# Kernel tuning notes

Measured on AMD Instinct MI355X. Metric: run time of the kernel, lower is better.

The kernel has to match this reference:

```python
import jax, jax.numpy as jnp
import numpy as np

D_MODEL = 2048
N_HEADS = 16
HEAD_DIM = D_MODEL // N_HEADS  # 128
HIDDEN = int(8 * D_MODEL / 3)  # 5461
EPS = 1e-6


def setup_inputs() -> dict:
    key = jax.random.key(0)
    ks = jax.random.split(key, 12)
    B, S = 2, 2048
    std = D_MODEL ** -0.5
    return {
        "x": jax.random.normal(ks[0], (B, S, D_MODEL), jnp.float32),
        "freq_cis": jax.random.normal(ks[1], (S, HEAD_DIM // 2, 2, 2), jnp.float32),
        "wq": jax.random.normal(ks[2], (D_MODEL, D_MODEL), jnp.float32) * std,
        "wk": jax.random.normal(ks[3], (D_MODEL, D_MODEL), jnp.float32) * std,
        "wv": jax.random.normal(ks[4], (D_MODEL, D_MODEL), jnp.float32) * std,
        "wo": jax.random.normal(ks[5], (D_MODEL, D_MODEL), jnp.float32) * std,
        "bo": jnp.zeros((D_MODEL,), jnp.float32),
        "w1": jax.random.normal(ks[6], (HIDDEN, D_MODEL), jnp.float32) * std,
        "w3": jax.random.normal(ks[7], (HIDDEN, D_MODEL), jnp.float32) * std,
        "w2": jax.random.normal(ks[8], (D_MODEL, HIDDEN), jnp.float32) * (HIDDEN ** -0.5),
        "g_attn": jnp.ones((D_MODEL,), jnp.float32),
        "g_ffn": jnp.ones((D_MODEL,), jnp.float32),
    }


def rmsnorm(x, g):
    xf = x.astype(jnp.float32)
    return xf * jax.lax.rsqrt(jnp.mean(xf * xf, axis=-1, keepdims=True) + EPS) * g


def rope(xq, xk, f):
    # xq/xk: [b, s, h, hd]; f: [s, hd/2, 2, 2]
    b, s, h, hd = xq.shape
    xq_ = xq.reshape(b, s, h, hd // 2, 2)
    xk_ = xk.reshape(b, s, h, hd // 2, 2)
    # out[b,s,h,i,j] = sum_k x[b,s,h,i,k] * f[s,i,j,k]
    q = jnp.einsum("bshik,sijk->bshij", xq_, f).reshape(b, s, h, hd)
    k = jnp.einsum("bshik,sijk->bshij", xk_, f).reshape(b, s, h, hd)
    return q, k


def reference(x, freq_cis, wq, wk, wv, wo, bo, w1, w3, w2, g_attn, g_ffn):
    b, s, d = x.shape
    h, hd = N_HEADS, HEAD_DIM
    scale = hd ** -0.5

    # --- attention sublayer ---
    xn = rmsnorm(x, g_attn)
    q = jnp.einsum("bsd,ed->bse", xn, wq).reshape(b, s, h, hd)
    k = jnp.einsum("bsd,ed->bse", xn, wk).reshape(b, s, h, hd)
    v = jnp.einsum("bsd,ed->bse", xn, wv).reshape(b, s, h, hd)
    q, k = rope(q, k, freq_cis[:s])
    attn = jnp.einsum("bqhd,bkhd->bhqk", q, k) * scale
    attn = jax.nn.softmax(attn, axis=-1)
    o = jnp.einsum("bhqk,bkhd->bqhd", attn, v).reshape(b, s, d)
    o = jnp.einsum("bsd,ed->bse", o, wo) + bo
    hres = x + o

    # --- SwiGLU FFN sublayer ---
    hn = rmsnorm(hres, g_ffn)
    x1 = jnp.einsum("bsd,hd->bsh", hn, w1)
    x3 = jnp.einsum("bsd,hd->bsh", hn, w3)
    ffn = jnp.einsum("bsh,dh->bsd", jax.nn.silu(x1) * x3, w2)
    return hres + ffn
```

## Files before the change

kernel.cpp:

```cpp
#include <hip/hip_runtime.h>

#define D_MODEL 2048
#define NHEADS 16
#define HDIM 128
#define HIDDEN_ 5461
#define HP2 5632
#define BATCH 2
#define SEQ 2048
#define MTOK 4096

typedef unsigned short u16;
typedef __attribute__((ext_vector_type(8))) short bf16x8;
typedef __attribute__((ext_vector_type(4))) float f32x4;
typedef __attribute__((ext_vector_type(4))) short s16x4;

__device__ __forceinline__ u16 f2b(float f) {
  union { float f; unsigned u; } v; v.f = f;
  return (u16)((v.u + 0x7FFFu + ((v.u >> 16) & 1u)) >> 16);
}
__device__ __forceinline__ float b2f(u16 u) {
  union { unsigned u; float f; } v; v.u = ((unsigned)u) << 16;
  return v.f;
}
__device__ __forceinline__ void gload16(const void* g, void* l) {
  __builtin_amdgcn_global_load_lds(
      (const __attribute__((address_space(1))) unsigned int*)g,
      (__attribute__((address_space(3))) unsigned int*)l, 16, 0, 0);
}

#define SB0() __builtin_amdgcn_sched_barrier(0)
#define BARRIER() do { SB0(); __builtin_amdgcn_s_barrier(); SB0(); } while (0)
#define LGKM0() do { asm volatile("s_waitcnt lgkmcnt(0)" ::: "memory"); SB0(); } while (0)

__global__ __launch_bounds__(256) void k_conv8(const float* __restrict__ src,
                                               u16* __restrict__ dst, int n8) {
  int stride = gridDim.x * 256;
  for (int i = blockIdx.x * 256 + threadIdx.x; i < n8; i += stride) {
    const float4* s = (const float4*)src + (size_t)i * 2;
    float4 a = s[0], b = s[1];
    bf16x8 o;
    o[0] = f2b(a.x); o[1] = f2b(a.y); o[2] = f2b(a.z); o[3] = f2b(a.w);
    o[4] = f2b(b.x); o[5] = f2b(b.y); o[6] = f2b(b.z); o[7] = f2b(b.w);
    ((bf16x8*)dst)[i] = o;
  }
}

__global__ __launch_bounds__(256) void k_conv3(const float* __restrict__ s0,
                                               const float* __restrict__ s1,
                                               const float* __restrict__ s2,
                                               u16* __restrict__ dst) {
  const int n8 = D_MODEL * D_MODEL / 8;
  int total = 3 * n8;
  int stride = gridDim.x * 256;
  for (int i = blockIdx.x * 256 + threadIdx.x; i < total; i += stride) {
    int seg = i >> 19, j = i & (n8 - 1);
    const float* s = (seg == 0) ? s0 : (seg == 1 ? s1 : s2);
    const float4* sp = (const float4*)s + (size_t)j * 2;
    float4 a = sp[0], b = sp[1];
    bf16x8 o;
    o[0] = f2b(a.x); o[1] = f2b(a.y); o[2] = f2b(a.z); o[3] = f2b(a.w);
    o[4] = f2b(b.x); o[5] = f2b(b.y); o[6] = f2b(b.z); o[7] = f2b(b.w);
    ((bf16x8*)dst)[i] = o;
  }
}

__global__ __launch_bounds__(256) void k_convw13(const float* __restrict__ w1,
                                                 const float* __restrict__ w3,
                                                 u16* __restrict__ dst) {
  const int n8 = (11264 * D_MODEL) / 8;
  int stride = gridDim.x * 256;
  for (int i = blockIdx.x * 256 + threadIdx.x; i < n8; i += stride) {
    int r = i >> 8, c8 = i & 255;
    int t = r & 255;
    int srow = ((r >> 8) << 7) + (t & 127);
    bf16x8 o;
    if (srow < HIDDEN_) {
      const float* s = (t < 128) ? w1 : w3;
      const float4* sp = (const float4*)(s + (size_t)srow * D_MODEL + c8 * 8);
      float4 a = sp[0], b = sp[1];
      o[0] = f2b(a.x); o[1] = f2b(a.y); o[2] = f2b(a.z); o[3] = f2b(a.w);
      o[4] = f2b(b.x); o[5] = f2b(b.y); o[6] = f2b(b.z); o[7] = f2b(b.w);
    } else {
      o = (bf16x8){0, 0, 0, 0, 0, 0, 0, 0};
    }
    ((bf16x8*)dst)[i] = o;
  }
}

__global__ __launch_bounds__(256) void k_convpad(const float* __restrict__ src,
                                                 u16* __restrict__ dst,
                                                 int srows, int scols, int drows, int dcols) {
  size_t n = (size_t)drows * dcols;
  size_t stride = (size_t)gridDim.x * 256;
  for (size_t i = blockIdx.x * 256 + threadIdx.x; i < n; i += stride) {
    int r = (int)(i / dcols), c = (int)(i % dcols);
    float v = (r < srows && c < scols) ? src[(size_t)r * scols + c] : 0.f;
    dst[i] = f2b(v);
  }
}

__global__ __launch_bounds__(256) void k_rmsnorm(const float* __restrict__ X,
                                                 const float* __restrict__ G,
                                                 u16* __restrict__ Out) {
  int row = blockIdx.x;
  int tid = threadIdx.x;
  const float4* x4 = (const float4*)(X + (size_t)row * D_MODEL);
  float4 a = x4[tid * 2], b = x4[tid * 2 + 1];
  float ss = a.x * a.x + a.y * a.y + a.z * a.z + a.w * a.w +
             b.x * b.x + b.y * b.y + b.z * b.z + b.w * b.w;
#pragma unroll
  for (int off = 1; off < 64; off <<= 1) ss += __shfl_xor(ss, off);
  __shared__ float part[4];
  if ((tid & 63) == 0) part[tid >> 6] = ss;
  __syncthreads();
  float rstd = rsqrtf((part[0] + part[1] + part[2] + part[3]) * (1.0f / D_MODEL) + 1e-6f);
  const float4* g4 = (const float4*)G;
  float4 ga = g4[tid * 2], gb = g4[tid * 2 + 1];
  bf16x8 o;
  o[0] = f2b(a.x * rstd * ga.x); o[1] = f2b(a.y * rstd * ga.y);
  o[2] = f2b(a.z * rstd * ga.z); o[3] = f2b(a.w * rstd * ga.w);
  o[4] = f2b(b.x * rstd * gb.x); o[5] = f2b(b.y * rstd * gb.y);
  o[6] = f2b(b.z * rstd * gb.z); o[7] = f2b(b.w * rstd * gb.w);
  *((bf16x8*)(Out + (size_t)row * D_MODEL) + tid) = o;
}

template <int WN, int EPI>
__global__ __launch_bounds__(512, 2) void k_gemm2(const u16* __restrict__ A,
                                                  const u16* __restrict__ Bw,
                                                  const u16* __restrict__ Bw2,
                                                  void* __restrict__ O0,
                                                  void* __restrict__ O1,
                                                  void* __restrict__ O2,
                                                  const float* __restrict__ bias,
                                                  const float* __restrict__ res,
                                                  const u16* __restrict__ aux,
                                                  int M, int N, int K) {
  constexpr int BN = WN * 64;
  constexpr int PB = BN * 64;
  __shared__ __align__(128) char lds[65536 + 4 * PB];
  const int tid = threadIdx.x;
  const int w = tid >> 6, lane = tid & 63;
  const int lo = lane & 15, hi = lane >> 4;
  const int wr = w >> 2, wc = w & 3;

  const int ntN = N / BN;
  const int nwg = gridDim.x * gridDim.y;
  const int flat = blockIdx.y * gridDim.x + blockIdx.x;
  const int swz = (flat & 7) * (nwg >> 3) + (flat >> 3);
  const int tm = swz / ntN, tn = swz % ntN;
  const int m0 = tm * 256, n0 = tn * BN;

  const u16* bbase;
  if (EPI == 5)
    bbase = (n0 < 5632) ? Bw + (size_t)n0 * K : Bw2 + (size_t)(n0 - 5632) * K;
  else
    bbase = Bw + (size_t)n0 * K;

  auto stA = [&](int nb, int kk, int k0) {
#pragma unroll
    for (int j = 0; j < 2; ++j) {
      int row = j * 128 + (tid >> 2);
      const u16* g = A + (size_t)(m0 + row) * K + k0 + kk * 32 + (tid & 3) * 8;
      gload16(g, lds + nb * 32768 + kk * 16384 + j * 8192 + tid * 16);
    }
  };
  auto stB = [&](int nb, int kk, int k0) {
#pragma unroll
    for (int j = 0; j < WN / 2; ++j) {
      int row = j * 128 + (tid >> 2);
      const u16* g = bbase + (size_t)row * K + k0 + kk * 32 + (tid & 3) * 8;
      gload16(g, lds + 65536 + nb * 2 * PB + kk * PB + j * 8192 + tid * 16);
    }
  };
  auto ldA = [&](int buf, int kk, int mf) {
    return *(const bf16x8*)(lds + buf * 32768 + kk * 16384 +
                            (wr * 128 + mf * 16 + lo) * 64 + hi * 16);
  };
  auto ldB = [&](int buf, int kk, int nf) {
    return *(const bf16x8*)(lds + 65536 + buf * 2 * PB + kk * PB +
                            (wc * (WN * 16) + nf * 16 + lo) * 64 + hi * 16);
  };
#define VMCNT_CONFIRM()                                             \
  do {                                                              \
    if constexpr (WN == 4)                                          \
      asm volatile("s_waitcnt vmcnt(4)" ::: "memory");              \
    else                                                            \
      asm volatile("s_waitcnt vmcnt(3)" ::: "memory");              \
    SB0();                                                          \
  } while (0)

  f32x4 acc[8][WN];
#pragma unroll
  for (int i = 0; i < 8; i++)
#pragma unroll
    for (int j = 0; j < WN; j++) acc[i][j] = (f32x4){0.f, 0.f, 0.f, 0.f};

  stA(0, 0, 0);
  stB(0, 0, 0);
  stA(0, 1, 0);
  stB(0, 1, 0);
  VMCNT_CONFIRM();
  BARRIER();

  const int KT = K / 64;
  for (int kt = 0; kt < KT; ++kt) {
    const int buf = kt & 1, nb = buf ^ 1;
    int kn = (kt + 1) * 64;
    if (kn >= K) kn = 0;
    bf16x8 aF[4], bF[WN];

#pragma unroll
    for (int i = 0; i < 4; i++) aF[i] = ldA(buf, 0, i);
#pragma unroll
    for (int j = 0; j < WN; j++) bF[j] = ldB(buf, 0, j);
    stA(nb, 0, kn);
    BARRIER();
    LGKM0();
    __builtin_amdgcn_s_setprio(1);
#pragma unroll
    for (int i = 0; i < 4; i++)
#pragma unroll
      for (int j = 0; j < WN; j++)
        acc[i][j] = __builtin_amdgcn_mfma_f32_16x16x32_bf16(aF[i], bF[j], acc[i][j], 0, 0, 0);
    __builtin_amdgcn_s_setprio(0);
    BARRIER();

#pragma unroll
    for (int i = 0; i < 4; i++) aF[i] = ldA(buf, 0, 4 + i);
    stB(nb, 0, kn);
    VMCNT_CONFIRM();
    BARRIER();
    LGKM0();
    __builtin_amdgcn_s_setprio(1);
#pragma unroll
    for (int i = 0; i < 4; i++)
#pragma unroll
      for (int j = 0; j < WN; j++)
        acc[4 + i][j] = __builtin_amdgcn_mfma_f32_16x16x32_bf16(aF[i], bF[j], acc[4 + i][j], 0, 0, 0);
    __builtin_amdgcn_s_setprio(0);
    BARRIER();

#pragma unroll
    for (int i = 0; i < 4; i++) aF[i] = ldA(buf, 1, i);
#pragma unroll
    for (int j = 0; j < WN; j++) bF[j] = ldB(buf, 1, j);
    stA(nb, 1, kn);
    BARRIER();
    LGKM0();
    __builtin_amdgcn_s_setprio(1);
#pragma unroll
    for (int i = 0; i < 4; i++)
#pragma unroll
      for (int j = 0; j < WN; j++)
        acc[i][j] = __builtin_amdgcn_mfma_f32_16x16x32_bf16(aF[i], bF[j], acc[i][j], 0, 0, 0);
    __builtin_amdgcn_s_setprio(0);
    BARRIER();

#pragma unroll
    for (int i = 0; i < 4; i++) aF[i] = ldA(buf, 1, 4 + i);
    stB(nb, 1, kn);
    VMCNT_CONFIRM();
    BARRIER();
    LGKM0();
    __builtin_amdgcn_s_setprio(1);
#pragma unroll
    for (int i = 0; i < 4; i++)
#pragma unroll
      for (int j = 0; j < WN; j++)
        acc[4 + i][j] = __builtin_amdgcn_mfma_f32_16x16x32_bf16(aF[i], bF[j], acc[4 + i][j], 0, 0, 0);
    __builtin_amdgcn_s_setprio(0);
    BARRIER();
  }

  if (EPI == 6) {
    u16* xls = (u16*)lds;
    if (wc >= 2) {
#pragma unroll
      for (int i = 0; i < 8; i++)
#pragma unroll
        for (int j = 0; j < WN; j++) {
          int col = (wc - 2) * 64 + j * 16 + lo;
#pragma unroll
          for (int r = 0; r < 4; r++) {
            int row = wr * 128 + i * 16 + hi * 4 + r;
            xls[row * 132 + col] = f2b(acc[i][j][r]);
          }
        }
    }
    BARRIER();
    if (wc < 2) {
      int c0 = n0 >> 1;
#pragma unroll
      for (int i = 0; i < 8; i++)
#pragma unroll
        for (int j = 0; j < WN; j++) {
          int colL = wc * 64 + j * 16 + lo;
#pragma unroll
          for (int r = 0; r < 4; r++) {
            int rowL = wr * 128 + i * 16 + hi * 4 + r;
            float v1 = acc[i][j][r];
            float v3 = b2f(xls[rowL * 132 + colL]);
            float sig = 1.f / (1.f + __expf(-v1));
            ((u16*)O0)[(size_t)(m0 + rowL) * 5632 + c0 + colL] = f2b(v1 * sig * v3);
          }
        }
    }
    return;
  }
  u16* qkvout = nullptr;
  int c0 = 0;
  if (EPI == 1) {
    int seg = n0 >> 11;
    qkvout = (u16*)(seg == 0 ? O0 : (seg == 1 ? O1 : O2));
    c0 = n0 & 2047;
  }
  u16* w13out = nullptr;
  int w13c0 = 0;
  if (EPI == 5) {
    w13out = (u16*)(n0 < 5632 ? O0 : O1);
    w13c0 = (n0 < 5632) ? n0 : n0 - 5632;
  }
#pragma unroll
  for (int i = 0; i < 8; i++) {
#pragma unroll
    for (int j = 0; j < WN; j++) {
      int colL = wc * (WN * 16) + j * 16 + lo;
#pragma unroll
      for (int r = 0; r < 4; r++) {
        int row = m0 + wr * 128 + i * 16 + hi * 4 + r;
        float v = acc[i][j][r];
        if (EPI == 0) {
          ((u16*)O0)[(size_t)row * N + n0 + colL] = f2b(v);
        } else if (EPI == 1) {
          qkvout[(size_t)row * 2048 + c0 + colL] = f2b(v);
        } else if (EPI == 2) {
          size_t idx = (size_t)row * N + n0 + colL;
          ((float*)O0)[idx] = v + bias[n0 + colL] + res[idx];
        } else if (EPI == 3) {
          size_t idx = (size_t)row * N + n0 + colL;
          ((float*)O0)[idx] = v + res[idx];
        } else if (EPI == 5) {
          w13out[(size_t)row * 5632 + w13c0 + colL] = f2b(v);
        }
      }
    }
  }
#undef VMCNT_CONFIRM
}

__global__ __launch_bounds__(256) void k_rope(u16* __restrict__ Qb, u16* __restrict__ Kb,
                                              const float* __restrict__ F) {
  int n = MTOK * (D_MODEL / 2);
  int stride = gridDim.x * 256;
  for (int t = blockIdx.x * 256 + threadIdx.x; t < n; t += stride) {
    int i = t & 63;
    int rest = t >> 6;
    int hh = rest & 15;
    int tok = rest >> 4;
    int s = tok & (SEQ - 1);
    float4 f = ((const float4*)F)[s * 64 + i];
    size_t off = (size_t)tok * D_MODEL + hh * HDIM + i * 2;
    float x0 = b2f(Qb[off]), x1 = b2f(Qb[off + 1]);
    Qb[off] = f2b(x0 * f.x + x1 * f.y);
    Qb[off + 1] = f2b(x0 * f.z + x1 * f.w);
    x0 = b2f(Kb[off]); x1 = b2f(Kb[off + 1]);
    Kb[off] = f2b(x0 * f.x + x1 * f.y);
    Kb[off + 1] = f2b(x0 * f.z + x1 * f.w);
  }
}

__global__ __launch_bounds__(256) void k_vt(const u16* __restrict__ V, u16* __restrict__ VT) {
  __shared__ u16 t[64][72];
  const int stile = blockIdx.x;
  const int bh = blockIdx.y;
  const int dz = blockIdx.z;
  const int b = bh >> 4, h = bh & 15;
  const int tok0 = b * SEQ + stile * 64;
  const int d0 = dz * 64;
  const int tid = threadIdx.x;
#pragma unroll
  for (int p = 0; p < 2; p++) {
    int idx = p * 256 + tid;
    int row = idx >> 3, seg = idx & 7;
    bf16x8 v = *(const bf16x8*)(V + (size_t)(tok0 + row) * D_MODEL + h * HDIM + d0 + seg * 8);
    *(bf16x8*)(&t[row][seg * 8]) = v;
  }
  __syncthreads();
#pragma unroll
  for (int p = 0; p < 2; p++) {
    int idx = p * 256 + tid;
    int dr = idx >> 3, seg = idx & 7;
    bf16x8 o;
#pragma unroll
    for (int e = 0; e < 8; e++) o[e] = t[seg * 8 + e][dr];
    *(bf16x8*)(VT + ((size_t)bh * HDIM + d0 + dr) * SEQ + stile * 64 + seg * 8) = o;
  }
}

__global__ __launch_bounds__(256) void k_flash4(const u16* __restrict__ Q,
                                                const u16* __restrict__ Kb,
                                                const u16* __restrict__ VT,
                                                u16* __restrict__ O) {
  __shared__ u16 Kt[64 * 128];
  __shared__ u16 Vt[128 * 64];
  __shared__ u16 Pl[4][2][16 * 72];
  const int tid = threadIdx.x;
  const int w = tid >> 6, lane = tid & 63;
  const int lo = lane & 15, hi = lane >> 4;
  const int qt = blockIdx.x, bh = blockIdx.y;
  const int b = bh >> 4, h = bh & 15;
  const size_t qrow0 = (size_t)b * SEQ + qt * 128 + w * 32;
  const float SC = 0.08838834764831845f * 1.4426950408889634f;

  bf16x8 aQ[2][4];
#pragma unroll
  for (int qg = 0; qg < 2; qg++)
#pragma unroll
    for (int kb = 0; kb < 4; kb++)
      aQ[qg][kb] = *(const bf16x8*)(Q + (qrow0 + qg * 16 + lo) * D_MODEL + h * HDIM + kb * 32 + hi * 8);

  float m_s[2] = {-3.0e38f, -3.0e38f}, l_s[2] = {0.f, 0.f};
  f32x4 oacc[2][8];
#pragma unroll
  for (int qg = 0; qg < 2; qg++)
#pragma unroll
    for (int d = 0; d < 8; d++) oacc[qg][d] = (f32x4){0.f, 0.f, 0.f, 0.f};

  const int krowL = tid >> 4;
  const int kslot = (tid & 15) ^ (krowL & 7);
  const int vrowL = tid >> 3;
  const int vslot = (tid & 7) ^ (vrowL & 7);
  const u16* Kbase = Kb + (size_t)b * SEQ * D_MODEL + h * HDIM;
  const u16* Vbase = VT + (size_t)bh * HDIM * SEQ;
  unsigned* Plw = (unsigned*)&Pl[w][0][0];

  bf16x8 kreg[4], vreg[4];
  auto issue = [&](int kt) {
#pragma unroll
    for (int t = 0; t < 4; t++) {
      int row = t * 16 + krowL;
      kreg[t] = *(const bf16x8*)(Kbase + (size_t)(kt * 64 + row) * D_MODEL + kslot * 8);
    }
#pragma unroll
    for (int t = 0; t < 4; t++) {
      int row = t * 32 + vrowL;
      vreg[t] = *(const bf16x8*)(Vbase + (size_t)row * SEQ + kt * 64 + vslot * 8);
    }
  };
  auto commit = [&]() {
#pragma unroll
    for (int t = 0; t < 4; t++)
      *(bf16x8*)((char*)Kt + t * 4096 + tid * 16) = kreg[t];
#pragma unroll
    for (int t = 0; t < 4; t++)
      *(bf16x8*)((char*)Vt + t * 4096 + tid * 16) = vreg[t];
  };

  issue(0);
  commit();
  BARRIER();

  const int NT = SEQ / 64;
  for (int kt = 0; kt < NT; kt++) {
    if (kt + 1 < NT) {
      issue(kt + 1);
      SB0();
    }

    f32x4 sf[2][4];
#pragma unroll
    for (int cb = 0; cb < 4; cb++) {
      bf16x8 kA[4];
#pragma unroll
      for (int kb = 0; kb < 4; kb++) {
        int ps = (kb * 4 + hi) ^ (lo & 7);
        kA[kb] = *(const bf16x8*)(Kt + (cb * 16 + lo) * 128 + ps * 8);
      }
#pragma unroll
      for (int qg = 0; qg < 2; qg++) {
        f32x4 s = (f32x4){0.f, 0.f, 0.f, 0.f};
#pragma unroll
        for (int kb = 0; kb < 4; kb++)
          s = __builtin_amdgcn_mfma_f32_16x16x32_bf16(kA[kb], aQ[qg][kb], s, 0, 0, 0);
        sf[qg][cb] = s;
      }
    }

    float tsc[2];
    bool ok = true;
#pragma unroll
    for (int qg = 0; qg < 2; qg++) {
      float t0 = fmaxf(fmaxf(sf[qg][0][0], sf[qg][0][1]), fmaxf(sf[qg][0][2], sf[qg][0][3]));
      float t1 = fmaxf(fmaxf(sf[qg][1][0], sf[qg][1][1]), fmaxf(sf[qg][1][2], sf[qg][1][3]));
      float t2 = fmaxf(fmaxf(sf[qg][2][0], sf[qg][2][1]), fmaxf(sf[qg][2][2], sf[qg][2][3]));
      float t3 = fmaxf(fmaxf(sf[qg][3][0], sf[qg][3][1]), fmaxf(sf[qg][3][2], sf[qg][3][3]));
      float t = fmaxf(fmaxf(t0, t1), fmaxf(t2, t3));
      t = fmaxf(t, __shfl_xor(t, 16));
      t = fmaxf(t, __shfl_xor(t, 32));
      tsc[qg] = t * SC;
      ok = ok && (tsc[qg] - m_s[qg] <= 11.5f);
    }
    bool skip = __all(ok);
#pragma unroll
    for (int qg = 0; qg < 2; qg++) {
      float mm = m_s[qg];
      if (!skip) {
        mm = fmaxf(m_s[qg], tsc[qg]);
        float alpha = exp2f(m_s[qg] - mm);
        l_s[qg] *= alpha;
#pragma unroll
        for (int d = 0; d < 8; d++) oacc[qg][d] *= alpha;
        m_s[qg] = mm;
      }
      float rs = 0.f;
#pragma unroll
      for (int cb = 0; cb < 4; cb++) {
        float p0 = exp2f(sf[qg][cb][0] * SC - mm);
        float p1 = exp2f(sf[qg][cb][1] * SC - mm);
        float p2 = exp2f(sf[qg][cb][2] * SC - mm);
        float p3 = exp2f(sf[qg][cb][3] * SC - mm);
        rs += (p0 + p1) + (p2 + p3);
        unsigned pk0, pk1;
        asm("v_cvt_pk_bf16_f32 %0, %1, %2" : "=v"(pk0) : "v"(p0), "v"(p1));
        asm("v_cvt_pk_bf16_f32 %0, %1, %2" : "=v"(pk1) : "v"(p2), "v"(p3));
        Plw[qg * 576 + lo * 36 + cb * 8 + hi * 2 + 0] = pk0;
        Plw[qg * 576 + lo * 36 + cb * 8 + hi * 2 + 1] = pk1;
      }
      rs += __shfl_xor(rs, 16);
      rs += __shfl_xor(rs, 32);
      l_s[qg] += rs;
    }
    LGKM0();

    bf16x8 aP[2][2];
#pragma unroll
    for (int qg = 0; qg < 2; qg++)
#pragma unroll
      for (int ks = 0; ks < 2; ks++)
        aP[qg][ks] = *(const bf16x8*)(&Pl[w][qg][lo * 72 + ks * 32 + hi * 8]);
#pragma unroll
    for (int db = 0; db < 8; db++) {
      bf16x8 vA[2];
#pragma unroll
      for (int ks = 0; ks < 2; ks++) {
        int ps = (ks * 4 + hi) ^ (lo & 7);
        vA[ks] = *(const bf16x8*)(Vt + (db * 16 + lo) * 64 + ps * 8);
      }
#pragma unroll
      for (int qg = 0; qg < 2; qg++)
#pragma unroll
        for (int ks = 0; ks < 2; ks++)
          oacc[qg][db] = __builtin_amdgcn_mfma_f32_16x16x32_bf16(vA[ks], aP[qg][ks], oacc[qg][db], 0, 0, 0);
    }

    if (kt + 1 < NT) {
      BARRIER();
      commit();
      BARRIER();
    }
  }

#pragma unroll
  for (int qg = 0; qg < 2; qg++) {
    float inv = 1.f / l_s[qg];
    size_t rowoff = (qrow0 + qg * 16 + lo) * D_MODEL + h * HDIM;
#pragma unroll
    for (int db = 0; db < 8; db++) {
      s16x4 o;
#pragma unroll
      for (int r = 0; r < 4; r++) o[r] = (short)f2b(oacc[qg][db][r] * inv);
      *(s16x4*)(O + rowoff + db * 16 + hi * 4) = o;
    }
  }
}

extern "C" void kernel_launch(void* const* d_in, const int* in_sizes, int n_in,
                              void* d_out, int out_size, void* d_ws, size_t ws_size,
                              hipStream_t stream) {
  (void)in_sizes; (void)n_in; (void)out_size; (void)ws_size;
  const float* x  = (const float*)d_in[0];
  const float* fc = (const float*)d_in[1];
  const float* wq = (const float*)d_in[2];
  const float* wk = (const float*)d_in[3];
  const float* wv = (const float*)d_in[4];
  const float* wo = (const float*)d_in[5];
  const float* bo = (const float*)d_in[6];
  const float* w1 = (const float*)d_in[7];
  const float* w3 = (const float*)d_in[8];
  const float* w2 = (const float*)d_in[9];
  const float* ga = (const float*)d_in[10];
  const float* gf = (const float*)d_in[11];
  float* out = (float*)d_out;

  char* p = (char*)d_ws;
  auto alloc = [&](size_t bytes) { char* r = p; p += (bytes + 255) & ~(size_t)255; return r; };
  u16* xn   = (u16*)alloc((size_t)MTOK * D_MODEL * 2);
  u16* qb   = (u16*)alloc((size_t)MTOK * D_MODEL * 2);
  u16* kb   = (u16*)alloc((size_t)MTOK * D_MODEL * 2);
  u16* vb   = (u16*)alloc((size_t)MTOK * D_MODEL * 2);
  u16* x1   = (u16*)alloc((size_t)MTOK * HP2 * 2);
  u16* w13i = (u16*)alloc((size_t)11264 * D_MODEL * 2);
  u16* wsl  = (u16*)alloc((size_t)3 * D_MODEL * D_MODEL * 2);
  u16* vbt = xn;
  u16* ob  = vb;
  u16* hn  = qb;

  k_rmsnorm<<<MTOK, 256, 0, stream>>>(x, ga, xn);
  k_conv3<<<1536, 256, 0, stream>>>(wq, wk, wv, wsl);
  k_gemm2<4, 1><<<dim3(6144 / 256, MTOK / 256), 512, 0, stream>>>(
      xn, wsl, nullptr, qb, kb, vb, nullptr, nullptr, nullptr, MTOK, 6144, D_MODEL);
  k_rope<<<1024, 256, 0, stream>>>(qb, kb, fc);
  k_vt<<<dim3(SEQ / 64, BATCH * NHEADS, 2), 256, 0, stream>>>(vb, vbt);
  dim3 gfl(SEQ / 128, BATCH * NHEADS);
  k_flash4<<<gfl, 256, 0, stream>>>(qb, kb, vbt, ob);
  k_conv8<<<1024, 256, 0, stream>>>(wo, wsl, D_MODEL * D_MODEL / 8);
  k_gemm2<2, 2><<<dim3(2048 / 128, MTOK / 256), 512, 0, stream>>>(
      ob, wsl, nullptr, out, nullptr, nullptr, bo, x, nullptr, MTOK, D_MODEL, D_MODEL);

  k_rmsnorm<<<MTOK, 256, 0, stream>>>(out, gf, hn);
  k_convw13<<<2048, 256, 0, stream>>>(w1, w3, w13i);
  k_gemm2<4, 6><<<dim3(11264 / 256, MTOK / 256), 512, 0, stream>>>(
      hn, w13i, nullptr, x1, nullptr, nullptr, nullptr, nullptr, nullptr, MTOK, 11264, D_MODEL);
  k_convpad<<<1024, 256, 0, stream>>>(w2, wsl, D_MODEL, HIDDEN_, D_MODEL, HP2);
  k_gemm2<2, 3><<<dim3(2048 / 128, MTOK / 256), 512, 0, stream>>>(
      x1, wsl, nullptr, out, nullptr, nullptr, nullptr, out, nullptr, MTOK, D_MODEL, HP2);
}
```

Before: 734.0 us.

## Interleave w1/w3 rows so SwiGLU epilogue pairs values in registers

The fused w1/w3 weight conversion now interleaves w1 and w3 rows at 16-row granularity per wave column, so that each wave's adjacent MFMA fragments hold matching w1 and w3 outputs. The SwiGLU epilogue then combines acc[jp] and acc[jp+1] directly in registers. This removes the LDS staging of the w3 half, the barrier, and the idle half of the waves in the epilogue. The unused EPI==5 split-output paths are also removed. The cost is a more intricate weight permutation that must match the MFMA fragment layout exactly.

```diff
diff --git a/kernel.cpp b/kernel.cpp
--- a/kernel.cpp
+++ b/kernel.cpp
@@ -71,11 +71,12 @@
   int stride = gridDim.x * 256;
   for (int i = blockIdx.x * 256 + threadIdx.x; i < n8; i += stride) {
     int r = i >> 8, c8 = i & 255;
-    int t = r & 255;
-    int srow = ((r >> 8) << 7) + (t & 127);
+    int g = r >> 8, rem = r & 255;
+    int wcb = rem >> 6, t = rem & 63, pp = t >> 4, ll = t & 15;
+    int srow = g * 128 + wcb * 32 + (pp >> 1) * 16 + ll;
     bf16x8 o;
     if (srow < HIDDEN_) {
-      const float* s = (t < 128) ? w1 : w3;
+      const float* s = (pp & 1) ? w3 : w1;
       const float4* sp = (const float4*)(s + (size_t)srow * D_MODEL + c8 * 8);
       float4 a = sp[0], b = sp[1];
       o[0] = f2b(a.x); o[1] = f2b(a.y); o[2] = f2b(a.z); o[3] = f2b(a.w);
@@ -150,11 +151,8 @@
   const int tm = swz / ntN, tn = swz % ntN;
   const int m0 = tm * 256, n0 = tn * BN;
 
-  const u16* bbase;
-  if (EPI == 5)
-    bbase = (n0 < 5632) ? Bw + (size_t)n0 * K : Bw2 + (size_t)(n0 - 5632) * K;
-  else
-    bbase = Bw + (size_t)n0 * K;
+  const u16* bbase = Bw + (size_t)n0 * K;
+  (void)Bw2;
 
   auto stA = [&](int nb, int kk, int k0) {
 #pragma unroll
@@ -273,37 +271,21 @@
   }
 
   if (EPI == 6) {
-    u16* xls = (u16*)lds;
-    if (wc >= 2) {
-#pragma unroll
-      for (int i = 0; i < 8; i++)
-#pragma unroll
-        for (int j = 0; j < WN; j++) {
-          int col = (wc - 2) * 64 + j * 16 + lo;
-#pragma unroll
-          for (int r = 0; r < 4; r++) {
-            int row = wr * 128 + i * 16 + hi * 4 + r;
-            xls[row * 132 + col] = f2b(acc[i][j][r]);
-          }
+    int c0 = n0 >> 1;
+#pragma unroll
+    for (int i = 0; i < 8; i++) {
+#pragma unroll
+      for (int jp = 0; jp < WN; jp += 2) {
+        int colL = wc * 32 + (jp >> 1) * 16 + lo;
+#pragma unroll
+        for (int r = 0; r < 4; r++) {
+          int row = m0 + wr * 128 + i * 16 + hi * 4 + r;
+          float v1 = acc[i][jp][r];
+          float v3 = acc[i][jp + 1][r];
+          float sig = 1.f / (1.f + __expf(-v1));
+          ((u16*)O0)[(size_t)row * 5632 + c0 + colL] = f2b(v1 * sig * v3);
         }
-    }
-    BARRIER();
-    if (wc < 2) {
-      int c0 = n0 >> 1;
-#pragma unroll
-      for (int i = 0; i < 8; i++)
-#pragma unroll
-        for (int j = 0; j < WN; j++) {
-          int colL = wc * 64 + j * 16 + lo;
-#pragma unroll
-          for (int r = 0; r < 4; r++) {
-            int rowL = wr * 128 + i * 16 + hi * 4 + r;
-            float v1 = acc[i][j][r];
-            float v3 = b2f(xls[rowL * 132 + colL]);
-            float sig = 1.f / (1.f + __expf(-v1));
-            ((u16*)O0)[(size_t)(m0 + rowL) * 5632 + c0 + colL] = f2b(v1 * sig * v3);
-          }
-        }
+      }
     }
     return;
   }
@@ -313,12 +295,6 @@
     int seg = n0 >> 11;
     qkvout = (u16*)(seg == 0 ? O0 : (seg == 1 ? O1 : O2));
     c0 = n0 & 2047;
-  }
-  u16* w13out = nullptr;
-  int w13c0 = 0;
-  if (EPI == 5) {
-    w13out = (u16*)(n0 < 5632 ? O0 : O1);
-    w13c0 = (n0 < 5632) ? n0 : n0 - 5632;
   }
 #pragma unroll
   for (int i = 0; i < 8; i++) {
@@ -339,8 +315,6 @@
         } else if (EPI == 3) {
           size_t idx = (size_t)row * N + n0 + colL;
           ((float*)O0)[idx] = v + res[idx];
-        } else if (EPI == 5) {
-          w13out[(size_t)row * 5632 + w13c0 + colL] = f2b(v);
         }
       }
     }
```

Measured after the change: 715.0 us. 2.6% less time.
